# Optimization experiments

Measured on AMD Instinct MI355X. Metric: run time of the kernel, lower is better.

Reference implementation:

```python
import jax, jax.numpy as jnp
import numpy as np

B, N, C = 8, 1374, 768
H = 12
HD = C // H  # 64
HIDDEN = int(C * 4.0)  # 3072
EPS = 1e-5


def setup_inputs() -> dict:
    key = jax.random.key(0)
    ks = jax.random.split(key, 12)
    s = 0.02
    return {
        "x": jax.random.normal(ks[0], (B, N, C), jnp.float32),
        "rope_freqs": jax.random.normal(ks[1], (1, N, 1, HD), jnp.float32),
        "ln1_g": jnp.ones((C,), jnp.float32),
        "ln1_b": jnp.zeros((C,), jnp.float32),
        "qkv_w": jax.random.normal(ks[2], (3 * C, C), jnp.float32) * s,
        "qkv_b": jnp.zeros((3 * C,), jnp.float32),
        "proj_w": jax.random.normal(ks[3], (C, C), jnp.float32) * s,
        "proj_b": jnp.zeros((C,), jnp.float32),
        "ln2_g": jnp.ones((C,), jnp.float32),
        "ln2_b": jnp.zeros((C,), jnp.float32),
        "w1": jax.random.normal(ks[4], (HIDDEN, C), jnp.float32) * s,
        "b1": jnp.zeros((HIDDEN,), jnp.float32),
        "w2": jax.random.normal(ks[5], (HIDDEN, C), jnp.float32) * s,
        "b2": jnp.zeros((HIDDEN,), jnp.float32),
        "w3": jax.random.normal(ks[6], (C, HIDDEN), jnp.float32) * s,
        "b3": jnp.zeros((C,), jnp.float32),
    }


def _layernorm(x, g, b):
    mu = jnp.mean(x, axis=-1, keepdims=True)
    var = jnp.mean(jnp.square(x - mu), axis=-1, keepdims=True)
    return (x - mu) * jax.lax.rsqrt(var + EPS) * g + b


def _rotate_half(x):
    x1, x2 = jnp.split(x, 2, axis=-1)
    return jnp.concatenate([-x2, x1], axis=-1)


def _apply_rope(q, k, freqs):
    # freqs: [1, N, 1, HD] -> [1, 1, N, HD] (matches torch permute(0,2,1,3))
    f = jnp.transpose(freqs, (0, 2, 1, 3))
    cos, sin = jnp.cos(f), jnp.sin(f)
    q_rot = q * cos + _rotate_half(q) * sin
    k_rot = k * cos + _rotate_half(k) * sin
    return q_rot, k_rot


def reference(x, rope_freqs, ln1_g, ln1_b, qkv_w, qkv_b, proj_w, proj_b,
              ln2_g, ln2_b, w1, b1, w2, b2, w3, b3):
    scale = HD ** -0.5
    # --- Attention branch ---
    h = _layernorm(x, ln1_g, ln1_b)
    qkv = jnp.einsum('bnc,dc->bnd', h, qkv_w) + qkv_b          # [B,N,3C]
    qkv = qkv.reshape(B, N, 3, H, HD).transpose(2, 0, 3, 1, 4)  # [3,B,H,N,HD]
    q, k, v = qkv[0], qkv[1], qkv[2]
    # rope_freqs covers all N tokens -> n_special = 0 path
    q, k = _apply_rope(q, k, rope_freqs)
    attn = jnp.einsum('bhnd,bhmd->bhnm', q, k) * scale          # [B,H,N,N]
    attn = jax.nn.softmax(attn, axis=-1)
    o = jnp.einsum('bhnm,bhmd->bhnd', attn, v)                  # [B,H,N,HD]
    o = o.transpose(0, 2, 1, 3).reshape(B, N, C)
    o = jnp.einsum('bnc,dc->bnd', o, proj_w) + proj_b
    x = x + o
    # --- SwiGLU MLP branch ---
    h2 = _layernorm(x, ln2_g, ln2_b)
    x1 = jnp.einsum('bnc,hc->bnh', h2, w1) + b1
    x2 = jnp.einsum('bnc,hc->bnh', h2, w2) + b2
    hid = jax.nn.silu(x1) * x2
    mlp_out = jnp.einsum('bnh,ch->bnc', hid, w3) + b3
    return x + mlp_out
```

## Files before the change

### kernel.cpp

```cpp
#include <hip/hip_runtime.h>
#include <stdint.h>

#define B_ 8
#define N_ 1374
#define C_ 768
#define H_ 12
#define HD_ 64
#define HID_ 3072
#define M_ (B_*N_)
#define MPAD_ 11008
#define QT_ 22
#define QT2_ 11

typedef __attribute__((ext_vector_type(8))) short short8;
typedef __attribute__((ext_vector_type(4))) float f32x4;
typedef __attribute__((ext_vector_type(4))) _Float16 half4;

__device__ __forceinline__ unsigned short f2bf(float f) {
  unsigned u = __float_as_uint(f);
  u += 0x7FFF + ((u >> 16) & 1);
  return (unsigned short)(u >> 16);
}
__device__ __forceinline__ float bf2f(unsigned short h) {
  return __uint_as_float(((unsigned)h) << 16);
}

#if __has_builtin(__builtin_amdgcn_global_load_lds)
#define HAVE_GLL 1
#endif

__device__ __forceinline__ void gld16(const unsigned short* g, unsigned short* l) {
#ifdef HAVE_GLL
  __builtin_amdgcn_global_load_lds((const __attribute__((address_space(1))) void*)g,
                                   (__attribute__((address_space(3))) void*)l, 16, 0, 0);
#else
  *(short8*)l = *(const short8*)g;
#endif
}

__global__ __launch_bounds__(256) void cvt5_kernel(
    const float* __restrict__ s0, const float* __restrict__ s1,
    const float* __restrict__ s2, const float* __restrict__ s3,
    const float* __restrict__ s4, unsigned short* __restrict__ out) {
  int id = blockIdx.x * 256 + threadIdx.x;
  const float* src; int off;
  if (id < 442368)        { src = s0; off = id; }
  else if (id < 589824)   { src = s1; off = id - 442368; }
  else if (id < 1179648)  { src = s2; off = id - 589824; }
  else if (id < 1769472)  { src = s3; off = id - 1179648; }
  else                    { src = s4; off = id - 1769472; }
  float4 v = ((const float4*)src)[off];
  ushort4 o;
  o.x = f2bf(v.x); o.y = f2bf(v.y); o.z = f2bf(v.z); o.w = f2bf(v.w);
  ((ushort4*)out)[id] = o;
}

__global__ __launch_bounds__(256) void ln_kernel(const float* __restrict__ in,
    const float* __restrict__ g, const float* __restrict__ bta,
    unsigned short* __restrict__ out) {
  int row = blockIdx.x;
  int t = threadIdx.x;
  const float* xr = in + (size_t)row * C_;
  float v0 = xr[t], v1 = xr[t + 256], v2 = xr[t + 512];
  float s1 = v0 + v1 + v2;
  float s2 = v0*v0 + v1*v1 + v2*v2;
  for (int off = 1; off < 64; off <<= 1) {
    s1 += __shfl_xor(s1, off, 64);
    s2 += __shfl_xor(s2, off, 64);
  }
  __shared__ float r1[4], r2[4];
  int wave = t >> 6, lane = t & 63;
  if (lane == 0) { r1[wave] = s1; r2[wave] = s2; }
  __syncthreads();
  float tot1 = r1[0] + r1[1] + r1[2] + r1[3];
  float tot2 = r2[0] + r2[1] + r2[2] + r2[3];
  float mu = tot1 * (1.0f / C_);
  float var = tot2 * (1.0f / C_) - mu * mu;
  float rs = rsqrtf(var + 1e-5f);
  size_t ob = (size_t)row * C_;
  out[ob + t]       = f2bf((v0 - mu) * rs * g[t]       + bta[t]);
  out[ob + t + 256] = f2bf((v1 - mu) * rs * g[t + 256] + bta[t + 256]);
  out[ob + t + 512] = f2bf((v2 - mu) * rs * g[t + 512] + bta[t + 512]);
}

template<int EPI, int ROPE, int TM, int SWZ>
__global__ __launch_bounds__(256, (TM == 64) ? 4 : 2) void gemm_bt(
    const unsigned short* __restrict__ A,
    const unsigned short* __restrict__ W,
    void* __restrict__ outp,
    const float* __restrict__ bias0,
    const float* __restrict__ resid,
    const float* __restrict__ freqs,
    int K, int ldo, int Mvalid, int X)
{
  constexpr int MI = TM / 32;
  __shared__ __align__(16) unsigned short As[2][TM * 32];
  __shared__ __align__(16) unsigned short Bs[2][4096];
  const int t = threadIdx.x;
  const int lane = t & 63;
  const int wave = t >> 6;
  const int wm = (wave >> 1) * (TM / 2);
  const int wn = (wave & 1) * 64;
  const int lr = lane & 15;
  const int lg = lane >> 4;
  const int lk = lg * 8;
  int bx, by;
  if (SWZ) {
    int Y = gridDim.x / X;
    int lin = blockIdx.x;
    int sgsz = X * 8;
    int sg = lin / sgsz;
    int base_y = sg * 8;
    int rows = Y - base_y; if (rows > 8) rows = 8;
    int within = lin - sg * sgsz;
    by = base_y + within % rows;
    bx = within / rows;
  } else {
    bx = blockIdx.x % X;
    by = blockIdx.x / X;
  }
  const int tm0 = by * TM;
  const int tn0 = bx * 128;
  const int r0 = t >> 2;
  const int c0 = (t & 3) * 8;
  const unsigned short* ga0 = A + (size_t)(tm0 + r0) * K + c0;
  const unsigned short* ga1 = A + (size_t)(tm0 + 64 + r0) * K + c0;
  const unsigned short* gb0 = W + (size_t)(tn0 + r0) * K + c0;
  const unsigned short* gb1 = W + (size_t)(tn0 + 64 + r0) * K + c0;
  f32x4 zero = {0.f, 0.f, 0.f, 0.f};
  f32x4 acc[MI][4];
#pragma unroll
  for (int mi = 0; mi < MI; ++mi)
#pragma unroll
    for (int ni = 0; ni < 4; ++ni) acc[mi][ni] = zero;

  for (int kt = 0; kt < K; kt += 64) {
    __syncthreads();
    gld16(ga0 + kt,      &As[0][t * 8]);
    gld16(ga0 + kt + 32, &As[1][t * 8]);
    if (TM == 128) {
      gld16(ga1 + kt,      &As[0][2048 + t * 8]);
      gld16(ga1 + kt + 32, &As[1][2048 + t * 8]);
    }
    gld16(gb0 + kt,      &Bs[0][t * 8]);
    gld16(gb1 + kt,      &Bs[0][2048 + t * 8]);
    gld16(gb0 + kt + 32, &Bs[1][t * 8]);
    gld16(gb1 + kt + 32, &Bs[1][2048 + t * 8]);
    __syncthreads();
#pragma unroll
    for (int u = 0; u < 2; ++u) {
      short8 af[MI], bfr[4];
#pragma unroll
      for (int mi = 0; mi < MI; ++mi) af[mi] = *(const short8*)&As[u][(wm + mi * 16 + lr) * 32 + lk];
#pragma unroll
      for (int ni = 0; ni < 4; ++ni) bfr[ni] = *(const short8*)&Bs[u][(wn + ni * 16 + lr) * 32 + lk];
#pragma unroll
      for (int mi = 0; mi < MI; ++mi)
#pragma unroll
        for (int ni = 0; ni < 4; ++ni)
          acc[mi][ni] = __builtin_amdgcn_mfma_f32_16x16x32_bf16(af[mi], bfr[ni], acc[mi][ni], 0, 0, 0);
    }
  }

  if (EPI == 0) {
    bool dorope = ROPE && ((tn0 + wn) < 1536);
#pragma unroll
    for (int mi = 0; mi < MI; ++mi) {
#pragma unroll
      for (int p = 0; p < 2; ++p) {
        int col1 = tn0 + wn + p * 16 + lr;
        int col2 = col1 + 32;
        float bv1 = bias0[col1], bv2 = bias0[col2];
        int e = p * 16 + lr;
#pragma unroll
        for (int r = 0; r < 4; ++r) {
          int row = tm0 + wm + mi * 16 + lg * 4 + r;
          float v1 = acc[mi][p][r] + bv1;
          float v2 = acc[mi][p + 2][r] + bv2;
          float o1 = v1, o2 = v2;
          if (dorope) {
            int n = row % N_;
            float f1 = freqs[n * HD_ + e];
            float f2 = freqs[n * HD_ + e + 32];
            float c1, s1, c2, s2;
            __sincosf(f1, &s1, &c1);
            __sincosf(f2, &s2, &c2);
            o1 = v1 * c1 - v2 * s1;
            o2 = v2 * c2 + v1 * s2;
          }
          size_t base = (size_t)row * ldo;
          ((unsigned short*)outp)[base + col1] = f2bf(o1);
          ((unsigned short*)outp)[base + col2] = f2bf(o2);
        }
      }
    }
  } else {
#pragma unroll
    for (int mi = 0; mi < MI; ++mi) {
#pragma unroll
      for (int ni = 0; ni < 4; ++ni) {
        int col = tn0 + wn + ni * 16 + lr;
        float bval = bias0[col];
#pragma unroll
        for (int r = 0; r < 4; ++r) {
          int row = tm0 + wm + mi * 16 + lg * 4 + r;
          float v = acc[mi][ni][r] + bval;
          size_t idx = (size_t)row * ldo + col;
          if (EPI == 1) {
            if (row < Mvalid) ((float*)outp)[idx] = resid[idx] + v;
          } else {
            if (row < Mvalid) ((float*)outp)[idx] = ((float*)outp)[idx] + v;
          }
        }
      }
    }
  }
}

__global__ __launch_bounds__(256, 2) void gemm_w12_swiglu(
    const unsigned short* __restrict__ A,
    const unsigned short* __restrict__ W1,
    const unsigned short* __restrict__ W2,
    unsigned short* __restrict__ hid,
    const float* __restrict__ b1,
    const float* __restrict__ b2)
{
  __shared__ __align__(16) unsigned short As[2][4096];
  __shared__ __align__(16) unsigned short B1s[2][2048];
  __shared__ __align__(16) unsigned short B2s[2][2048];
  const int t = threadIdx.x;
  const int lane = t & 63;
  const int wave = t >> 6;
  const int wm = (wave >> 1) * 64;
  const int wn = (wave & 1) * 32;
  const int lr = lane & 15;
  const int lg = lane >> 4;
  const int lk = lg * 8;
  const int tm0 = blockIdx.y * 128;
  const int tn0 = blockIdx.x * 64;
  const int r0 = t >> 2;
  const int c0 = (t & 3) * 8;
  const unsigned short* ga0 = A + (size_t)(tm0 + r0) * 768 + c0;
  const unsigned short* ga1 = A + (size_t)(tm0 + 64 + r0) * 768 + c0;
  const unsigned short* g1 = W1 + (size_t)(tn0 + r0) * 768 + c0;
  const unsigned short* g2 = W2 + (size_t)(tn0 + r0) * 768 + c0;
  f32x4 zero = {0.f, 0.f, 0.f, 0.f};
  f32x4 acc1[4][2], acc2[4][2];
#pragma unroll
  for (int mi = 0; mi < 4; ++mi)
#pragma unroll
    for (int ni = 0; ni < 2; ++ni) { acc1[mi][ni] = zero; acc2[mi][ni] = zero; }

  for (int kt = 0; kt < 768; kt += 64) {
    __syncthreads();
    gld16(ga0 + kt,      &As[0][t * 8]);
    gld16(ga1 + kt,      &As[0][2048 + t * 8]);
    gld16(ga0 + kt + 32, &As[1][t * 8]);
    gld16(ga1 + kt + 32, &As[1][2048 + t * 8]);
    gld16(g1 + kt,       &B1s[0][t * 8]);
    gld16(g1 + kt + 32,  &B1s[1][t * 8]);
    gld16(g2 + kt,       &B2s[0][t * 8]);
    gld16(g2 + kt + 32,  &B2s[1][t * 8]);
    __syncthreads();
#pragma unroll
    for (int u = 0; u < 2; ++u) {
      short8 af[4], b1f[2], b2f[2];
#pragma unroll
      for (int mi = 0; mi < 4; ++mi) af[mi] = *(const short8*)&As[u][(wm + mi * 16 + lr) * 32 + lk];
#pragma unroll
      for (int ni = 0; ni < 2; ++ni) {
        b1f[ni] = *(const short8*)&B1s[u][(wn + ni * 16 + lr) * 32 + lk];
        b2f[ni] = *(const short8*)&B2s[u][(wn + ni * 16 + lr) * 32 + lk];
      }
#pragma unroll
      for (int mi = 0; mi < 4; ++mi)
#pragma unroll
        for (int ni = 0; ni < 2; ++ni) {
          acc1[mi][ni] = __builtin_amdgcn_mfma_f32_16x16x32_bf16(af[mi], b1f[ni], acc1[mi][ni], 0, 0, 0);
          acc2[mi][ni] = __builtin_amdgcn_mfma_f32_16x16x32_bf16(af[mi], b2f[ni], acc2[mi][ni], 0, 0, 0);
        }
    }
  }
#pragma unroll
  for (int mi = 0; mi < 4; ++mi) {
#pragma unroll
    for (int ni = 0; ni < 2; ++ni) {
      int col = tn0 + wn + ni * 16 + lr;
      float bv1 = b1[col], bv2 = b2[col];
#pragma unroll
      for (int r = 0; r < 4; ++r) {
        int row = tm0 + wm + mi * 16 + lg * 4 + r;
        float a1 = acc1[mi][ni][r] + bv1;
        float a2 = acc2[mi][ni][r] + bv2;
        float h = a1 / (1.f + __expf(-a1)) * a2;
        hid[(size_t)row * HID_ + col] = f2bf(h);
      }
    }
  }
}

__global__ __launch_bounds__(256, 2) void attn_kernel(
    const unsigned short* __restrict__ qkv,
    unsigned short* __restrict__ o2)
{
  __shared__ __align__(16) unsigned short Ks[64 * 80];
  __shared__ __align__(16) _Float16 Vt[64 * 72];
  int bidx = blockIdx.x;
  int qt = bidx % QT2_;
  int bh = bidx / QT2_;
  int head = bh % H_;
  int b = bh / H_;
  int t = threadIdx.x, lane = t & 63, wave = t >> 6;
  int lr = lane & 15, lg = lane >> 4;

  short8 bq[2][2];
#pragma unroll
  for (int s = 0; s < 2; ++s) {
    int m = qt * 128 + wave * 32 + s * 16 + lr;
    int mc = (m < N_) ? m : (N_ - 1);
    const unsigned short* qrow = qkv + (size_t)(b * N_ + mc) * 2304 + head * HD_;
    bq[s][0] = *(const short8*)(qrow + lg * 8);
    bq[s][1] = *(const short8*)(qrow + 32 + lg * 8);
  }

  f32x4 zero = {0.f, 0.f, 0.f, 0.f};
  f32x4 acc[2][4];
#pragma unroll
  for (int s = 0; s < 2; ++s)
#pragma unroll
    for (int dt = 0; dt < 4; ++dt) acc[s][dt] = zero;
  float den[2] = {0.f, 0.f};

  const int vp = t & 31;
  const int vc = t >> 5;

  for (int jt = 0; jt < QT_; ++jt) {
    __syncthreads();
#pragma unroll
    for (int u = t; u < 512; u += 256) {
      int row = u >> 3, c = u & 7;
      int j = jt * 64 + row;
      int jc = (j < N_) ? j : (N_ - 1);
      const unsigned short* src = qkv + (size_t)(b * N_ + jc) * 2304 + 768 + head * HD_ + c * 8;
      *(short8*)&Ks[row * 80 + c * 8] = *(const short8*)src;
    }
    {
      int j0 = jt * 64 + 2 * vp;
      int j1 = j0 + 1;
      int j0c = (j0 < N_) ? j0 : (N_ - 1);
      int j1c = (j1 < N_) ? j1 : (N_ - 1);
      const unsigned short* s0 = qkv + (size_t)(b * N_ + j0c) * 2304 + 1536 + head * HD_ + vc * 8;
      const unsigned short* s1 = qkv + (size_t)(b * N_ + j1c) * 2304 + 1536 + head * HD_ + vc * 8;
      short8 v0 = *(const short8*)s0;
      short8 v1 = *(const short8*)s1;
#pragma unroll
      for (int i = 0; i < 8; ++i) {
        _Float16 lo = (_Float16)bf2f((unsigned short)v0[i]);
        _Float16 hi = (_Float16)bf2f((unsigned short)v1[i]);
        unsigned w = (unsigned)__builtin_bit_cast(unsigned short, lo)
                   | ((unsigned)__builtin_bit_cast(unsigned short, hi) << 16);
        *(unsigned*)&Vt[(vc * 8 + i) * 72 + 2 * vp] = w;
      }
    }
    __syncthreads();
#pragma unroll
    for (int st = 0; st < 4; ++st) {
      short8 ak0 = *(const short8*)&Ks[(st * 16 + lr) * 80 + lg * 8];
      short8 ak1 = *(const short8*)&Ks[(st * 16 + lr) * 80 + 32 + lg * 8];
      int jb = jt * 64 + st * 16 + lg * 4;
      half4 pf[2];
#pragma unroll
      for (int s = 0; s < 2; ++s) {
        f32x4 sc = zero;
        sc = __builtin_amdgcn_mfma_f32_16x16x32_bf16(ak0, bq[s][0], sc, 0, 0, 0);
        sc = __builtin_amdgcn_mfma_f32_16x16x32_bf16(ak1, bq[s][1], sc, 0, 0, 0);
        float dsum = 0.f;
#pragma unroll
        for (int r = 0; r < 4; ++r) {
          float pv = (jb + r < N_) ? __expf(sc[r] * 0.125f) : 0.f;
          dsum += pv;
          pf[s][r] = (_Float16)pv;
        }
        den[s] += dsum;
      }
#pragma unroll
      for (int dt = 0; dt < 4; ++dt) {
        half4 bv = *(const half4*)&Vt[(dt * 16 + lr) * 72 + st * 16 + lg * 4];
        acc[0][dt] = __builtin_amdgcn_mfma_f32_16x16x16f16(pf[0], bv, acc[0][dt], 0, 0, 0);
        acc[1][dt] = __builtin_amdgcn_mfma_f32_16x16x16f16(pf[1], bv, acc[1][dt], 0, 0, 0);
      }
    }
  }
#pragma unroll
  for (int s = 0; s < 2; ++s) {
    den[s] += __shfl_xor(den[s], 16, 64);
    den[s] += __shfl_xor(den[s], 32, 64);
  }
#pragma unroll
  for (int s = 0; s < 2; ++s) {
#pragma unroll
    for (int r = 0; r < 4; ++r) {
      float dm = __shfl(den[s], lg * 4 + r, 64);
      int m = qt * 128 + wave * 32 + s * 16 + lg * 4 + r;
      if (m < N_) {
        float invd = 1.f / dm;
        unsigned short* orow = o2 + (size_t)(b * N_ + m) * C_ + head * HD_;
#pragma unroll
        for (int dt = 0; dt < 4; ++dt)
          orow[dt * 16 + lr] = f2bf(acc[s][dt][r] * invd);
      }
    }
  }
}

extern "C" void kernel_launch(void* const* d_in, const int* in_sizes, int n_in,
                              void* d_out, int out_size, void* d_ws, size_t ws_size,
                              hipStream_t stream) {
  const float* x      = (const float*)d_in[0];
  const float* freqs  = (const float*)d_in[1];
  const float* ln1_g  = (const float*)d_in[2];
  const float* ln1_b  = (const float*)d_in[3];
  const float* qkv_w  = (const float*)d_in[4];
  const float* qkv_b  = (const float*)d_in[5];
  const float* proj_w = (const float*)d_in[6];
  const float* proj_b = (const float*)d_in[7];
  const float* ln2_g  = (const float*)d_in[8];
  const float* ln2_b  = (const float*)d_in[9];
  const float* w1     = (const float*)d_in[10];
  const float* b1     = (const float*)d_in[11];
  const float* w2     = (const float*)d_in[12];
  const float* b2     = (const float*)d_in[13];
  const float* w3     = (const float*)d_in[14];
  const float* b3     = (const float*)d_in[15];
  float* out = (float*)d_out;
  char* ws = (char*)d_ws;

  unsigned short* hB     = (unsigned short*)(ws + 0);
  unsigned short* wqkvB  = (unsigned short*)(ws + 16908288);
  unsigned short* wprojB = (unsigned short*)(ws + 20447232);
  unsigned short* w12B   = (unsigned short*)(ws + 21626880);
  unsigned short* w3B    = (unsigned short*)(ws + 31064064);
  unsigned short* qkvB   = (unsigned short*)(ws + 35782656);
  unsigned short* o2B    = (unsigned short*)(ws + 86507520);
  unsigned short* hidB   = qkvB;

  cvt5_kernel<<<9216, 256, 0, stream>>>(qkv_w, proj_w, w1, w2, w3, wqkvB);

  ln_kernel<<<M_, 256, 0, stream>>>(x, ln1_g, ln1_b, hB);
  gemm_bt<0, 1, 128, 1><<<18 * 86, 256, 0, stream>>>(hB, wqkvB, qkvB, qkv_b, nullptr, freqs, 768, 2304, M_, 18);
  attn_kernel<<<B_ * H_ * QT2_, 256, 0, stream>>>(qkvB, o2B);
  gemm_bt<1, 0, 64, 1><<<6 * 172, 256, 0, stream>>>(o2B, wprojB, out, proj_b, x, nullptr, 768, 768, M_, 6);

  ln_kernel<<<M_, 256, 0, stream>>>(out, ln2_g, ln2_b, hB);
  gemm_w12_swiglu<<<dim3(48, 86), 256, 0, stream>>>(hB, w12B, w12B + 3072 * 768, hidB, b1, b2);
  gemm_bt<3, 0, 64, 1><<<6 * 172, 256, 0, stream>>>(hidB, w3B, out, b3, nullptr, nullptr, 3072, 768, M_, 6);
}
```

Baseline: 556.9 us.

## Double attention query tile per block and use exp2 with packed fp16 conversion

The attention kernel now handles 256 query rows per block (64 per wave) instead of 128, so each K/V tile loaded into LDS is reused across twice as many queries. The grid shrinks to 576 blocks, and block indices are remapped so that a block's batch-head index is taken from the low bits. Softmax exponentials now use exp2f with a folded log2e scale, and fp16 packing uses cvt_pkrtz. In exchange, register pressure rises (accumulators double), fewer blocks are available for parallelism, and the last query tile wastes more padded rows.

```diff
diff --git a/kernel.cpp b/kernel.cpp
--- a/kernel.cpp
+++ b/kernel.cpp
@@ -10,11 +10,12 @@
 #define M_ (B_*N_)
 #define MPAD_ 11008
 #define QT_ 22
-#define QT2_ 11
+#define QT3_ 6
 
 typedef __attribute__((ext_vector_type(8))) short short8;
 typedef __attribute__((ext_vector_type(4))) float f32x4;
 typedef __attribute__((ext_vector_type(4))) _Float16 half4;
+typedef __fp16 pk16x2 __attribute__((ext_vector_type(2)));
 
 __device__ __forceinline__ unsigned short f2bf(float f) {
   unsigned u = __float_as_uint(f);
@@ -305,18 +306,20 @@
 {
   __shared__ __align__(16) unsigned short Ks[64 * 80];
   __shared__ __align__(16) _Float16 Vt[64 * 72];
-  int bidx = blockIdx.x;
-  int qt = bidx % QT2_;
-  int bh = bidx / QT2_;
+  int lin = blockIdx.x;
+  int x = lin & 7, y = lin >> 3;
+  int bh = x * 12 + y / QT3_;
+  int qt = y % QT3_;
   int head = bh % H_;
   int b = bh / H_;
   int t = threadIdx.x, lane = t & 63, wave = t >> 6;
   int lr = lane & 15, lg = lane >> 4;
-
-  short8 bq[2][2];
-#pragma unroll
-  for (int s = 0; s < 2; ++s) {
-    int m = qt * 128 + wave * 32 + s * 16 + lr;
+  const float expC = 0.18033688011112042f;
+
+  short8 bq[4][2];
+#pragma unroll
+  for (int s = 0; s < 4; ++s) {
+    int m = qt * 256 + wave * 64 + s * 16 + lr;
     int mc = (m < N_) ? m : (N_ - 1);
     const unsigned short* qrow = qkv + (size_t)(b * N_ + mc) * 2304 + head * HD_;
     bq[s][0] = *(const short8*)(qrow + lg * 8);
@@ -324,12 +327,12 @@
   }
 
   f32x4 zero = {0.f, 0.f, 0.f, 0.f};
-  f32x4 acc[2][4];
-#pragma unroll
-  for (int s = 0; s < 2; ++s)
+  f32x4 acc[4][4];
+#pragma unroll
+  for (int s = 0; s < 4; ++s)
 #pragma unroll
     for (int dt = 0; dt < 4; ++dt) acc[s][dt] = zero;
-  float den[2] = {0.f, 0.f};
+  float den[4] = {0.f, 0.f, 0.f, 0.f};
 
   const int vp = t & 31;
   const int vc = t >> 5;
@@ -355,11 +358,9 @@
       short8 v1 = *(const short8*)s1;
 #pragma unroll
       for (int i = 0; i < 8; ++i) {
-        _Float16 lo = (_Float16)bf2f((unsigned short)v0[i]);
-        _Float16 hi = (_Float16)bf2f((unsigned short)v1[i]);
-        unsigned w = (unsigned)__builtin_bit_cast(unsigned short, lo)
-                   | ((unsigned)__builtin_bit_cast(unsigned short, hi) << 16);
-        *(unsigned*)&Vt[(vc * 8 + i) * 72 + 2 * vp] = w;
+        pk16x2 pk = __builtin_amdgcn_cvt_pkrtz(bf2f((unsigned short)v0[i]),
+                                               bf2f((unsigned short)v1[i]));
+        *(unsigned*)&Vt[(vc * 8 + i) * 72 + 2 * vp] = __builtin_bit_cast(unsigned, pk);
       }
     }
     __syncthreads();
@@ -368,40 +369,42 @@
       short8 ak0 = *(const short8*)&Ks[(st * 16 + lr) * 80 + lg * 8];
       short8 ak1 = *(const short8*)&Ks[(st * 16 + lr) * 80 + 32 + lg * 8];
       int jb = jt * 64 + st * 16 + lg * 4;
-      half4 pf[2];
-#pragma unroll
-      for (int s = 0; s < 2; ++s) {
+      half4 pf[4];
+#pragma unroll
+      for (int s = 0; s < 4; ++s) {
         f32x4 sc = zero;
         sc = __builtin_amdgcn_mfma_f32_16x16x32_bf16(ak0, bq[s][0], sc, 0, 0, 0);
         sc = __builtin_amdgcn_mfma_f32_16x16x32_bf16(ak1, bq[s][1], sc, 0, 0, 0);
-        float dsum = 0.f;
-#pragma unroll
-        for (int r = 0; r < 4; ++r) {
-          float pv = (jb + r < N_) ? __expf(sc[r] * 0.125f) : 0.f;
-          dsum += pv;
-          pf[s][r] = (_Float16)pv;
-        }
-        den[s] += dsum;
+        float pv0 = (jb + 0 < N_) ? exp2f(sc[0] * expC) : 0.f;
+        float pv1 = (jb + 1 < N_) ? exp2f(sc[1] * expC) : 0.f;
+        float pv2 = (jb + 2 < N_) ? exp2f(sc[2] * expC) : 0.f;
+        float pv3 = (jb + 3 < N_) ? exp2f(sc[3] * expC) : 0.f;
+        den[s] += (pv0 + pv1) + (pv2 + pv3);
+        pk16x2 lo = __builtin_amdgcn_cvt_pkrtz(pv0, pv1);
+        pk16x2 hi = __builtin_amdgcn_cvt_pkrtz(pv2, pv3);
+        pf[s][0] = (_Float16)lo[0]; pf[s][1] = (_Float16)lo[1];
+        pf[s][2] = (_Float16)hi[0]; pf[s][3] = (_Float16)hi[1];
       }
 #pragma unroll
       for (int dt = 0; dt < 4; ++dt) {
         half4 bv = *(const half4*)&Vt[(dt * 16 + lr) * 72 + st * 16 + lg * 4];
-        acc[0][dt] = __builtin_amdgcn_mfma_f32_16x16x16f16(pf[0], bv, acc[0][dt], 0, 0, 0);
-        acc[1][dt] = __builtin_amdgcn_mfma_f32_16x16x16f16(pf[1], bv, acc[1][dt], 0, 0, 0);
-      }
-    }
-  }
-#pragma unroll
-  for (int s = 0; s < 2; ++s) {
+#pragma unroll
+        for (int s = 0; s < 4; ++s)
+          acc[s][dt] = __builtin_amdgcn_mfma_f32_16x16x16f16(pf[s], bv, acc[s][dt], 0, 0, 0);
+      }
+    }
+  }
+#pragma unroll
+  for (int s = 0; s < 4; ++s) {
     den[s] += __shfl_xor(den[s], 16, 64);
     den[s] += __shfl_xor(den[s], 32, 64);
   }
 #pragma unroll
-  for (int s = 0; s < 2; ++s) {
+  for (int s = 0; s < 4; ++s) {
 #pragma unroll
     for (int r = 0; r < 4; ++r) {
       float dm = __shfl(den[s], lg * 4 + r, 64);
-      int m = qt * 128 + wave * 32 + s * 16 + lg * 4 + r;
+      int m = qt * 256 + wave * 64 + s * 16 + lg * 4 + r;
       if (m < N_) {
         float invd = 1.f / dm;
         unsigned short* orow = o2 + (size_t)(b * N_ + m) * C_ + head * HD_;
@@ -448,7 +451,7 @@
 
   ln_kernel<<<M_, 256, 0, stream>>>(x, ln1_g, ln1_b, hB);
   gemm_bt<0, 1, 128, 1><<<18 * 86, 256, 0, stream>>>(hB, wqkvB, qkvB, qkv_b, nullptr, freqs, 768, 2304, M_, 18);
-  attn_kernel<<<B_ * H_ * QT2_, 256, 0, stream>>>(qkvB, o2B);
+  attn_kernel<<<B_ * H_ * QT3_, 256, 0, stream>>>(qkvB, o2B);
   gemm_bt<1, 0, 64, 1><<<6 * 172, 256, 0, stream>>>(o2B, wprojB, out, proj_b, x, nullptr, 768, 768, M_, 6);
 
   ln_kernel<<<M_, 256, 0, stream>>>(out, ln2_g, ln2_b, hB);
```

Result: slower. 595.0 us (+6.8%).
